# Kernel tuning notes

Measured on AMD Instinct MI355X. Metric: run time of the kernel, lower is better.

## Reference

```python
import jax, jax.numpy as jnp
import numpy as np
import math

HEAD = 4

def _neighbors3x3(t):
    # t: [b, g, d, h, w] -> [b, g, d, 9, h, w], zero-padded 3x3 neighborhoods
    b, g, d, h, w = t.shape
    tp = jnp.pad(t, ((0, 0), (0, 0), (0, 0), (1, 1), (1, 1)))
    # torch.nn.Unfold(kernel_size=3) ordering: kernel positions row-major (dy, dx)
    patches = [tp[:, :, :, dy:dy + h, dx:dx + w] for dy in range(3) for dx in range(3)]
    return jnp.stack(patches, axis=3)


def setup_inputs() -> dict:
    key = jax.random.key(0)
    k1, k2 = jax.random.split(key)
    x = jax.random.normal(k1, (8, 128, 96, 96), dtype=jnp.float32)
    # 1x1 conv weight, no bias: [out=3*out_features, in=in_features]
    W_trans = jax.random.normal(k2, (384, 128), dtype=jnp.float32) * 0.05
    return {"x": x, "W_trans": W_trans}


def reference(x, W_trans):
    b, cin, h, w = x.shape
    # 1x1 conv == channel GEMM
    t = jnp.einsum('bchw,oc->bohw', x, W_trans)  # [b, 3*C, h, w]
    q, k, v = jnp.split(t, 3, axis=1)            # each [b, C, h, w]
    C = q.shape[1]
    d = C // HEAD
    q = q.reshape(b, HEAD, d, h, w)
    k = k.reshape(b, HEAD, d, h, w)
    v = v.reshape(b, HEAD, d, h, w)
    kn = _neighbors3x3(k)  # [b, g, d, 9, h, w]
    vn = _neighbors3x3(v)  # [b, g, d, 9, h, w]
    # att[b,g,n,h,w] = <q[b,g,:,h,w], kn[b,g,:,n,h,w]> / sqrt(d)
    att = jnp.einsum('bgdhw,bgdnhw->bgnhw', q, kn) / math.sqrt(d)
    att = jax.nn.softmax(att, axis=2)
    # dropout p=0.4 is identity in eval mode
    out = jnp.einsum('bgnhw,bgdnhw->bgdhw', att, vn)  # [b, g, d, h, w]
    return out.reshape(b, C, h, w)
```

## Files before the change

### kernel.cpp

```cpp
#include <hip/hip_runtime.h>

#define NB     8
#define CIN    128
#define HEADS  4
#define DHEAD  32
#define HDIM   96
#define WDIM   96
#define HW     9216
#define TP     64

typedef __bf16 bf16x8 __attribute__((ext_vector_type(8)));
typedef float  f32x4  __attribute__((ext_vector_type(4)));

__device__ __forceinline__ unsigned f2bf(float f) {
  unsigned u = __float_as_uint(f);
  return (u + 0x7fffu + ((u >> 16) & 1u)) >> 16;
}
__device__ __forceinline__ unsigned pack2(float a, float b) {
  return f2bf(a) | (f2bf(b) << 16);
}
__device__ __forceinline__ float bflo(unsigned u) { return __uint_as_float(u << 16); }
__device__ __forceinline__ float bfhi(unsigned u) { return __uint_as_float(u & 0xffff0000u); }

__global__ __launch_bounds__(256) void wpack_kernel(const float* __restrict__ W,
                                                    uint4* __restrict__ Wf) {
  const int u = blockIdx.x * 256 + threadIdx.x;
  const int lane = u & 63, kb = (u >> 6) & 3, ot = u >> 8;
  const int o = ot * 16 + (lane & 15);
  const int c0 = kb * 32 + (lane >> 4) * 8;
  const float4* w = (const float4*)(W + (size_t)o * CIN + c0);
  float4 w0 = w[0], w1 = w[1];
  uint4 r;
  r.x = pack2(w0.x, w0.y); r.y = pack2(w0.z, w0.w);
  r.z = pack2(w1.x, w1.y); r.w = pack2(w1.z, w1.w);
  Wf[u] = r;
}

__global__ __launch_bounds__(256) void qkv_kernel(const float* __restrict__ x,
                                                  const uint4* __restrict__ Wf,
                                                  unsigned short* __restrict__ qkvb) {
  __shared__ uint4 xs[16 * 64];
  const int b  = blockIdx.y;
  const int p0 = blockIdx.x * TP;
  const int t  = threadIdx.x;

  {
    const int p = t & 63, cg_hi = t >> 6;
    const int pt = p >> 4, n = p & 15;
    const float* xb = x + (size_t)b * CIN * HW + p0 + p;
#pragma unroll
    for (int i = 0; i < 4; ++i) {
      const int cg = i * 4 + cg_hi;
      const int c0 = cg * 8;
      const int kb = cg >> 2, q = cg & 3;
      float f[8];
#pragma unroll
      for (int j = 0; j < 8; ++j) f[j] = xb[(size_t)(c0 + j) * HW];
      uint4 r;
      r.x = pack2(f[0], f[1]); r.y = pack2(f[2], f[3]);
      r.z = pack2(f[4], f[5]); r.w = pack2(f[6], f[7]);
      xs[(pt * 4 + kb) * 64 + q * 16 + n] = r;
    }
  }
  __syncthreads();

  const int wv = t >> 6, lane = t & 63;
  const int colp = lane & 15, quad = lane >> 4;
#pragma unroll 1
  for (int it = 0; it < 6; ++it) {
    const int ot = wv * 6 + it;
    bf16x8 afrag[4];
#pragma unroll
    for (int kb = 0; kb < 4; ++kb) {
      uint4 tmp = Wf[(ot * 4 + kb) * 64 + lane];
      afrag[kb] = *(bf16x8*)&tmp;
    }
    const int o0 = ot * 16 + quad * 4;
    const int which = o0 >> 7, g = (o0 & 127) >> 5, d0 = o0 & 31;
    unsigned short* dst = qkvb
        + (((size_t)(which * NB + b) * HEADS + g) * HW) * DHEAD + d0;
#pragma unroll
    for (int pt = 0; pt < 4; ++pt) {
      f32x4 acc = {0.f, 0.f, 0.f, 0.f};
#pragma unroll
      for (int kb = 0; kb < 4; ++kb) {
        bf16x8 bfrag = *(bf16x8*)&xs[(pt * 4 + kb) * 64 + lane];
        acc = __builtin_amdgcn_mfma_f32_16x16x32_bf16(afrag[kb], bfrag, acc, 0, 0, 0);
      }
      const int pp = p0 + pt * 16 + colp;
      uint2 st;
      st.x = pack2(acc[0], acc[1]);
      st.y = pack2(acc[2], acc[3]);
      *(uint2*)(dst + (size_t)pp * DHEAD) = st;
    }
  }
}

__global__ __launch_bounds__(256) void attn_kernel(const unsigned short* __restrict__ qkvb,
                                                   float* __restrict__ out) {
  const int bg = blockIdx.z;
  const int h  = blockIdx.y * 8 + threadIdx.y;
  const int w  = blockIdx.x * 32 + threadIdx.x;
  const int b  = bg >> 2, g = bg & 3;

  const size_t plane = (size_t)HW * DHEAD;
  const uint4* Qb = (const uint4*)(qkvb + (size_t)bg * plane);
  const uint4* Kb = (const uint4*)(qkvb + (size_t)(32 + bg) * plane);
  const uint4* Vb = (const uint4*)(qkvb + (size_t)(64 + bg) * plane);
  const int p = h * WDIM + w;

  float q[32];
#pragma unroll
  for (int i = 0; i < 4; ++i) {
    uint4 u = Qb[p * 4 + i];
    q[i * 8 + 0] = bflo(u.x); q[i * 8 + 1] = bfhi(u.x);
    q[i * 8 + 2] = bflo(u.y); q[i * 8 + 3] = bfhi(u.y);
    q[i * 8 + 4] = bflo(u.z); q[i * 8 + 5] = bfhi(u.z);
    q[i * 8 + 6] = bflo(u.w); q[i * 8 + 7] = bfhi(u.w);
  }

  float att[9];
#pragma unroll
  for (int nn = 0; nn < 9; ++nn) {
    const int dy = nn / 3 - 1, dx = nn % 3 - 1;
    const int hh = h + dy, ww = w + dx;
    float dot = 0.0f;
    if (hh >= 0 && hh < HDIM && ww >= 0 && ww < WDIM) {
      const int pn = hh * WDIM + ww;
#pragma unroll
      for (int i = 0; i < 4; ++i) {
        uint4 u = Kb[pn * 4 + i];
        dot = fmaf(q[i * 8 + 0], bflo(u.x), dot);
        dot = fmaf(q[i * 8 + 1], bfhi(u.x), dot);
        dot = fmaf(q[i * 8 + 2], bflo(u.y), dot);
        dot = fmaf(q[i * 8 + 3], bfhi(u.y), dot);
        dot = fmaf(q[i * 8 + 4], bflo(u.z), dot);
        dot = fmaf(q[i * 8 + 5], bfhi(u.z), dot);
        dot = fmaf(q[i * 8 + 6], bflo(u.w), dot);
        dot = fmaf(q[i * 8 + 7], bfhi(u.w), dot);
      }
      dot *= 0.17677669529663687f;
    }
    att[nn] = dot;
  }

  float m = att[0];
#pragma unroll
  for (int nn = 1; nn < 9; ++nn) m = fmaxf(m, att[nn]);
  float s = 0.0f;
#pragma unroll
  for (int nn = 0; nn < 9; ++nn) { att[nn] = __expf(att[nn] - m); s += att[nn]; }
  const float inv = 1.0f / s;

  float acc[32];
#pragma unroll
  for (int i = 0; i < 32; ++i) acc[i] = 0.0f;
#pragma unroll
  for (int nn = 0; nn < 9; ++nn) {
    const int dy = nn / 3 - 1, dx = nn % 3 - 1;
    const int hh = h + dy, ww = w + dx;
    if (hh >= 0 && hh < HDIM && ww >= 0 && ww < WDIM) {
      const float wn = att[nn] * inv;
      const int pn = hh * WDIM + ww;
#pragma unroll
      for (int i = 0; i < 4; ++i) {
        uint4 u = Vb[pn * 4 + i];
        acc[i * 8 + 0] = fmaf(wn, bflo(u.x), acc[i * 8 + 0]);
        acc[i * 8 + 1] = fmaf(wn, bfhi(u.x), acc[i * 8 + 1]);
        acc[i * 8 + 2] = fmaf(wn, bflo(u.y), acc[i * 8 + 2]);
        acc[i * 8 + 3] = fmaf(wn, bfhi(u.y), acc[i * 8 + 3]);
        acc[i * 8 + 4] = fmaf(wn, bflo(u.z), acc[i * 8 + 4]);
        acc[i * 8 + 5] = fmaf(wn, bfhi(u.z), acc[i * 8 + 5]);
        acc[i * 8 + 6] = fmaf(wn, bflo(u.w), acc[i * 8 + 6]);
        acc[i * 8 + 7] = fmaf(wn, bfhi(u.w), acc[i * 8 + 7]);
      }
    }
  }

  float* ob = out + ((size_t)b * CIN + (size_t)g * DHEAD) * HW + p;
#pragma unroll
  for (int i = 0; i < 32; ++i) ob[(size_t)i * HW] = acc[i];
}

extern "C" void kernel_launch(void* const* d_in, const int* in_sizes, int n_in,
                              void* d_out, int out_size, void* d_ws, size_t ws_size,
                              hipStream_t stream) {
  (void)in_sizes; (void)n_in; (void)out_size; (void)ws_size;
  const float* x = (const float*)d_in[0];
  const float* W = (const float*)d_in[1];
  float* out = (float*)d_out;

  const size_t qkv_ushorts = (size_t)3 * NB * HEADS * HW * DHEAD;
  unsigned short* qkvb = (unsigned short*)d_ws;
  uint4* Wf = (uint4*)((char*)d_ws + qkv_ushorts * 2);

  wpack_kernel<<<24, 256, 0, stream>>>(W, Wf);
  qkv_kernel<<<dim3(HW / TP, NB), 256, 0, stream>>>(x, Wf, qkvb);
  attn_kernel<<<dim3(WDIM / 32, HDIM / 8, NB * HEADS), dim3(32, 8, 1), 0, stream>>>(qkvb, out);
}
```

Measured before the change: 127.7 us.

## Split head dim across lane halves in attention and shrink QKV pixel tile

The attention kernel now gives each pixel two threads, one per half of the 32-wide head dimension. The partial q·k dot products are combined with a cross-lane xor shuffle, and neighbour bounds checks become clamped addresses with masking. This halves per-thread registers and doubles thread count, raising occupancy and memory parallelism, at the cost of an extra shuffle and redundant softmax work. The QKV GEMM kernel halves its pixel tile to 32, giving twice as many blocks and smaller shared memory, and fully unrolls the output-tile loop, which may reduce weight-fragment reuse.

```diff
diff --git a/kernel.cpp b/kernel.cpp
--- a/kernel.cpp
+++ b/kernel.cpp
@@ -7,7 +7,7 @@
 #define HDIM   96
 #define WDIM   96
 #define HW     9216
-#define TP     64
+#define TP     32
 
 typedef __bf16 bf16x8 __attribute__((ext_vector_type(8)));
 typedef float  f32x4  __attribute__((ext_vector_type(4)));
@@ -39,34 +39,31 @@
 __global__ __launch_bounds__(256) void qkv_kernel(const float* __restrict__ x,
                                                   const uint4* __restrict__ Wf,
                                                   unsigned short* __restrict__ qkvb) {
-  __shared__ uint4 xs[16 * 64];
+  __shared__ uint4 xs[8 * 64];
   const int b  = blockIdx.y;
   const int p0 = blockIdx.x * TP;
   const int t  = threadIdx.x;
 
-  {
-    const int p = t & 63, cg_hi = t >> 6;
-    const int pt = p >> 4, n = p & 15;
-    const float* xb = x + (size_t)b * CIN * HW + p0 + p;
-#pragma unroll
-    for (int i = 0; i < 4; ++i) {
-      const int cg = i * 4 + cg_hi;
-      const int c0 = cg * 8;
-      const int kb = cg >> 2, q = cg & 3;
-      float f[8];
-#pragma unroll
-      for (int j = 0; j < 8; ++j) f[j] = xb[(size_t)(c0 + j) * HW];
-      uint4 r;
-      r.x = pack2(f[0], f[1]); r.y = pack2(f[2], f[3]);
-      r.z = pack2(f[4], f[5]); r.w = pack2(f[6], f[7]);
-      xs[(pt * 4 + kb) * 64 + q * 16 + n] = r;
-    }
+#pragma unroll
+  for (int i = 0; i < 2; ++i) {
+    const int slot = i * 256 + t;
+    const int px = slot & 31, oct = slot >> 5;
+    const int c0 = oct * 8;
+    const float* xb = x + ((size_t)b * CIN + c0) * HW + p0 + px;
+    float f[8];
+#pragma unroll
+    for (int j = 0; j < 8; ++j) f[j] = xb[(size_t)j * HW];
+    uint4 r;
+    r.x = pack2(f[0], f[1]); r.y = pack2(f[2], f[3]);
+    r.z = pack2(f[4], f[5]); r.w = pack2(f[6], f[7]);
+    const int pt = px >> 4, n = px & 15, kb = oct >> 2, q = oct & 3;
+    xs[(pt * 4 + kb) * 64 + q * 16 + n] = r;
   }
   __syncthreads();
 
   const int wv = t >> 6, lane = t & 63;
   const int colp = lane & 15, quad = lane >> 4;
-#pragma unroll 1
+#pragma unroll
   for (int it = 0; it < 6; ++it) {
     const int ot = wv * 6 + it;
     bf16x8 afrag[4];
@@ -80,7 +77,7 @@
     unsigned short* dst = qkvb
         + (((size_t)(which * NB + b) * HEADS + g) * HW) * DHEAD + d0;
 #pragma unroll
-    for (int pt = 0; pt < 4; ++pt) {
+    for (int pt = 0; pt < 2; ++pt) {
       f32x4 acc = {0.f, 0.f, 0.f, 0.f};
 #pragma unroll
       for (int kb = 0; kb < 4; ++kb) {
@@ -98,88 +95,98 @@
 
 __global__ __launch_bounds__(256) void attn_kernel(const unsigned short* __restrict__ qkvb,
                                                    float* __restrict__ out) {
+  const int tx = threadIdx.x;
+  const int wq = tx & 31, dh = tx >> 5;
+  const int w  = blockIdx.x * 32 + wq;
+  const int h  = blockIdx.y * 4 + threadIdx.y;
   const int bg = blockIdx.z;
-  const int h  = blockIdx.y * 8 + threadIdx.y;
-  const int w  = blockIdx.x * 32 + threadIdx.x;
   const int b  = bg >> 2, g = bg & 3;
 
   const size_t plane = (size_t)HW * DHEAD;
-  const uint4* Qb = (const uint4*)(qkvb + (size_t)bg * plane);
-  const uint4* Kb = (const uint4*)(qkvb + (size_t)(32 + bg) * plane);
-  const uint4* Vb = (const uint4*)(qkvb + (size_t)(64 + bg) * plane);
+  const unsigned short* Qb = qkvb + (size_t)bg * plane;
+  const unsigned short* Kb = qkvb + (size_t)(32 + bg) * plane;
+  const unsigned short* Vb = qkvb + (size_t)(64 + bg) * plane;
   const int p = h * WDIM + w;
 
-  float q[32];
-#pragma unroll
-  for (int i = 0; i < 4; ++i) {
-    uint4 u = Qb[p * 4 + i];
-    q[i * 8 + 0] = bflo(u.x); q[i * 8 + 1] = bfhi(u.x);
-    q[i * 8 + 2] = bflo(u.y); q[i * 8 + 3] = bfhi(u.y);
-    q[i * 8 + 4] = bflo(u.z); q[i * 8 + 5] = bfhi(u.z);
-    q[i * 8 + 6] = bflo(u.w); q[i * 8 + 7] = bfhi(u.w);
+  float q[16];
+  {
+    const uint4* qp = (const uint4*)(Qb + (size_t)p * DHEAD + dh * 16);
+    uint4 u0 = qp[0], u1 = qp[1];
+    q[0] = bflo(u0.x); q[1] = bfhi(u0.x); q[2] = bflo(u0.y); q[3] = bfhi(u0.y);
+    q[4] = bflo(u0.z); q[5] = bfhi(u0.z); q[6] = bflo(u0.w); q[7] = bfhi(u0.w);
+    q[8]  = bflo(u1.x); q[9]  = bfhi(u1.x); q[10] = bflo(u1.y); q[11] = bfhi(u1.y);
+    q[12] = bflo(u1.z); q[13] = bfhi(u1.z); q[14] = bflo(u1.w); q[15] = bfhi(u1.w);
   }
 
   float att[9];
 #pragma unroll
-  for (int nn = 0; nn < 9; ++nn) {
-    const int dy = nn / 3 - 1, dx = nn % 3 - 1;
-    const int hh = h + dy, ww = w + dx;
-    float dot = 0.0f;
-    if (hh >= 0 && hh < HDIM && ww >= 0 && ww < WDIM) {
-      const int pn = hh * WDIM + ww;
-#pragma unroll
-      for (int i = 0; i < 4; ++i) {
-        uint4 u = Kb[pn * 4 + i];
-        dot = fmaf(q[i * 8 + 0], bflo(u.x), dot);
-        dot = fmaf(q[i * 8 + 1], bfhi(u.x), dot);
-        dot = fmaf(q[i * 8 + 2], bflo(u.y), dot);
-        dot = fmaf(q[i * 8 + 3], bfhi(u.y), dot);
-        dot = fmaf(q[i * 8 + 4], bflo(u.z), dot);
-        dot = fmaf(q[i * 8 + 5], bfhi(u.z), dot);
-        dot = fmaf(q[i * 8 + 6], bflo(u.w), dot);
-        dot = fmaf(q[i * 8 + 7], bfhi(u.w), dot);
-      }
-      dot *= 0.17677669529663687f;
-    }
-    att[nn] = dot;
+  for (int dy = -1; dy <= 1; ++dy) {
+    const int hh = h + dy;
+    const int hc = min(max(hh, 0), HDIM - 1);
+    const bool rowOK = (unsigned)hh < (unsigned)HDIM;
+#pragma unroll
+    for (int dx = -1; dx <= 1; ++dx) {
+      const int nn = (dy + 1) * 3 + (dx + 1);
+      const int ww = w + dx;
+      const int wc = min(max(ww, 0), WDIM - 1);
+      const bool ok = rowOK && ((unsigned)ww < (unsigned)WDIM);
+      const int pn = hc * WDIM + wc;
+      const uint4* kp = (const uint4*)(Kb + (size_t)pn * DHEAD + dh * 16);
+      uint4 k0 = kp[0], k1 = kp[1];
+      float dot = 0.f;
+      dot = fmaf(q[0], bflo(k0.x), dot);  dot = fmaf(q[1], bfhi(k0.x), dot);
+      dot = fmaf(q[2], bflo(k0.y), dot);  dot = fmaf(q[3], bfhi(k0.y), dot);
+      dot = fmaf(q[4], bflo(k0.z), dot);  dot = fmaf(q[5], bfhi(k0.z), dot);
+      dot = fmaf(q[6], bflo(k0.w), dot);  dot = fmaf(q[7], bfhi(k0.w), dot);
+      dot = fmaf(q[8],  bflo(k1.x), dot); dot = fmaf(q[9],  bfhi(k1.x), dot);
+      dot = fmaf(q[10], bflo(k1.y), dot); dot = fmaf(q[11], bfhi(k1.y), dot);
+      dot = fmaf(q[12], bflo(k1.z), dot); dot = fmaf(q[13], bfhi(k1.z), dot);
+      dot = fmaf(q[14], bflo(k1.w), dot); dot = fmaf(q[15], bfhi(k1.w), dot);
+      dot += __shfl_xor(dot, 32);
+      att[nn] = ok ? dot * 0.17677669529663687f : 0.f;
+    }
   }
 
   float m = att[0];
 #pragma unroll
   for (int nn = 1; nn < 9; ++nn) m = fmaxf(m, att[nn]);
-  float s = 0.0f;
+  float s = 0.f;
 #pragma unroll
   for (int nn = 0; nn < 9; ++nn) { att[nn] = __expf(att[nn] - m); s += att[nn]; }
   const float inv = 1.0f / s;
 
-  float acc[32];
-#pragma unroll
-  for (int i = 0; i < 32; ++i) acc[i] = 0.0f;
-#pragma unroll
-  for (int nn = 0; nn < 9; ++nn) {
-    const int dy = nn / 3 - 1, dx = nn % 3 - 1;
-    const int hh = h + dy, ww = w + dx;
-    if (hh >= 0 && hh < HDIM && ww >= 0 && ww < WDIM) {
-      const float wn = att[nn] * inv;
-      const int pn = hh * WDIM + ww;
-#pragma unroll
-      for (int i = 0; i < 4; ++i) {
-        uint4 u = Vb[pn * 4 + i];
-        acc[i * 8 + 0] = fmaf(wn, bflo(u.x), acc[i * 8 + 0]);
-        acc[i * 8 + 1] = fmaf(wn, bfhi(u.x), acc[i * 8 + 1]);
-        acc[i * 8 + 2] = fmaf(wn, bflo(u.y), acc[i * 8 + 2]);
-        acc[i * 8 + 3] = fmaf(wn, bfhi(u.y), acc[i * 8 + 3]);
-        acc[i * 8 + 4] = fmaf(wn, bflo(u.z), acc[i * 8 + 4]);
-        acc[i * 8 + 5] = fmaf(wn, bfhi(u.z), acc[i * 8 + 5]);
-        acc[i * 8 + 6] = fmaf(wn, bflo(u.w), acc[i * 8 + 6]);
-        acc[i * 8 + 7] = fmaf(wn, bfhi(u.w), acc[i * 8 + 7]);
-      }
-    }
-  }
-
-  float* ob = out + ((size_t)b * CIN + (size_t)g * DHEAD) * HW + p;
-#pragma unroll
-  for (int i = 0; i < 32; ++i) ob[(size_t)i * HW] = acc[i];
+  float acc[16];
+#pragma unroll
+  for (int i = 0; i < 16; ++i) acc[i] = 0.f;
+#pragma unroll
+  for (int dy = -1; dy <= 1; ++dy) {
+    const int hh = h + dy;
+    const int hc = min(max(hh, 0), HDIM - 1);
+    const bool rowOK = (unsigned)hh < (unsigned)HDIM;
+#pragma unroll
+    for (int dx = -1; dx <= 1; ++dx) {
+      const int nn = (dy + 1) * 3 + (dx + 1);
+      const int ww = w + dx;
+      const int wc = min(max(ww, 0), WDIM - 1);
+      const bool ok = rowOK && ((unsigned)ww < (unsigned)WDIM);
+      const int pn = hc * WDIM + wc;
+      const float wn = ok ? att[nn] * inv : 0.f;
+      const uint4* vp = (const uint4*)(Vb + (size_t)pn * DHEAD + dh * 16);
+      uint4 v0 = vp[0], v1 = vp[1];
+      acc[0] = fmaf(wn, bflo(v0.x), acc[0]);  acc[1] = fmaf(wn, bfhi(v0.x), acc[1]);
+      acc[2] = fmaf(wn, bflo(v0.y), acc[2]);  acc[3] = fmaf(wn, bfhi(v0.y), acc[3]);
+      acc[4] = fmaf(wn, bflo(v0.z), acc[4]);  acc[5] = fmaf(wn, bfhi(v0.z), acc[5]);
+      acc[6] = fmaf(wn, bflo(v0.w), acc[6]);  acc[7] = fmaf(wn, bfhi(v0.w), acc[7]);
+      acc[8]  = fmaf(wn, bflo(v1.x), acc[8]);  acc[9]  = fmaf(wn, bfhi(v1.x), acc[9]);
+      acc[10] = fmaf(wn, bflo(v1.y), acc[10]); acc[11] = fmaf(wn, bfhi(v1.y), acc[11]);
+      acc[12] = fmaf(wn, bflo(v1.z), acc[12]); acc[13] = fmaf(wn, bfhi(v1.z), acc[13]);
+      acc[14] = fmaf(wn, bflo(v1.w), acc[14]); acc[15] = fmaf(wn, bfhi(v1.w), acc[15]);
+    }
+  }
+
+  float* ob = out + ((size_t)b * CIN + (size_t)g * DHEAD + dh * 16) * HW + p;
+#pragma unroll
+  for (int i = 0; i < 16; ++i) ob[(size_t)i * HW] = acc[i];
 }
 
 extern "C" void kernel_launch(void* const* d_in, const int* in_sizes, int n_in,
@@ -196,5 +203,5 @@
 
   wpack_kernel<<<24, 256, 0, stream>>>(W, Wf);
   qkv_kernel<<<dim3(HW / TP, NB), 256, 0, stream>>>(x, Wf, qkvb);
-  attn_kernel<<<dim3(WDIM / 32, HDIM / 8, NB * HEADS), dim3(32, 8, 1), 0, stream>>>(qkvb, out);
-}
+  attn_kernel<<<dim3(WDIM / 32, HDIM / 4, NB * HEADS), dim3(64, 4, 1), 0, stream>>>(qkvb, out);
+}
```

Result: no change. 128.4 us (+0.5%).
